# Kernel optimization log

Measured on AMD Instinct MI355X. Metric: run time of the kernel, lower is better.

The kernel has to match this reference:

```python
import jax, jax.numpy as jnp
import numpy as np

N_NODES = 50000
N_EDGES = 600000
NFEAT = 128
HIDDEN = 64
NCLASS = 40


def sage_conv(x, src, dst, Wl, bl, Wr, num_nodes):
    # PyG SAGEConv (aggr='mean'): out = lin_l(mean_{j->i} x_j) + lin_r(x_i)
    msg = x[src]                                                  # [E, d]
    agg = jax.ops.segment_sum(msg, dst, num_segments=num_nodes)   # [N, d]
    cnt = jax.ops.segment_sum(jnp.ones((src.shape[0],), x.dtype), dst,
                              num_segments=num_nodes)             # [N]
    agg = agg / jnp.maximum(cnt, 1.0)[:, None]
    return agg @ Wl.T + bl + x @ Wr.T


def setup_inputs() -> dict:
    key = jax.random.key(0)
    ks = jax.random.split(key, 8)
    x = jax.random.normal(ks[0], (N_NODES, NFEAT), dtype=jnp.float32)
    edge_index = jax.random.randint(ks[1], (2, N_EDGES), 0, N_NODES, dtype=jnp.int64)
    def glorot(k, shape):
        lim = np.sqrt(6.0 / (shape[0] + shape[1]))
        return jax.random.uniform(k, shape, jnp.float32, -lim, lim)
    Wl1 = glorot(ks[2], (HIDDEN, NFEAT))
    bl1 = jnp.zeros((HIDDEN,), jnp.float32)
    Wr1 = glorot(ks[3], (HIDDEN, NFEAT))
    Wl2 = glorot(ks[4], (NCLASS, HIDDEN))
    bl2 = jnp.zeros((NCLASS,), jnp.float32)
    Wr2 = glorot(ks[5], (NCLASS, HIDDEN))
    return {"x": x, "edge_index": edge_index, "Wl1": Wl1, "bl1": bl1,
            "Wr1": Wr1, "Wl2": Wl2, "bl2": bl2, "Wr2": Wr2}


def reference(x, edge_index, Wl1, bl1, Wr1, Wl2, bl2, Wr2):
    src, dst = edge_index[0], edge_index[1]
    h = sage_conv(x, src, dst, Wl1, bl1, Wr1, N_NODES)   # [N, 64]
    h = jax.nn.sigmoid(h)
    out = sage_conv(h, src, dst, Wl2, bl2, Wr2, N_NODES)  # [N, nclass]
    return out
```

## Files before the change

### kernel.cpp

```cpp
#include <hip/hip_runtime.h>
#include <cmath>

#define NN 50000
#define NE 600000
#define NF 128
#define NH 64
#define NC 40

#define SCAN_TPB 512
#define SCAN_NBLK 98

#define LDSP1 65
#define LDSP2 41

__global__ __launch_bounds__(256) void k_hist(const int* __restrict__ dst,
                                              int* __restrict__ deg) {
  int i0 = blockIdx.x * blockDim.x + threadIdx.x;
  int stride = gridDim.x * blockDim.x;
  for (int e = i0; e < NE; e += stride) atomicAdd(&deg[dst[e]], 1);
}

__global__ __launch_bounds__(SCAN_TPB) void k_scan1(const int* __restrict__ deg,
                                                    int* __restrict__ blocksum) {
  __shared__ int sd[SCAN_TPB];
  int i = blockIdx.x * SCAN_TPB + threadIdx.x;
  sd[threadIdx.x] = (i < NN) ? deg[i] : 0;
  __syncthreads();
  for (int off = SCAN_TPB / 2; off > 0; off >>= 1) {
    if (threadIdx.x < off) sd[threadIdx.x] += sd[threadIdx.x + off];
    __syncthreads();
  }
  if (threadIdx.x == 0) blocksum[blockIdx.x] = sd[0];
}

__global__ __launch_bounds__(128) void k_scan2(const int* __restrict__ blocksum,
                                               int* __restrict__ blockoff) {
  __shared__ int sd[128];
  int tid = threadIdx.x;
  int v = (tid < SCAN_NBLK) ? blocksum[tid] : 0;
  sd[tid] = v;
  __syncthreads();
  for (int off = 1; off < 128; off <<= 1) {
    int t = (tid >= off) ? sd[tid - off] : 0;
    __syncthreads();
    sd[tid] += t;
    __syncthreads();
  }
  if (tid < SCAN_NBLK) blockoff[tid] = sd[tid] - v;
}

__global__ __launch_bounds__(SCAN_TPB) void k_scan3(
    const int* __restrict__ deg, const int* __restrict__ blockoff,
    int* __restrict__ rowptr, int* __restrict__ cursor) {
  __shared__ int sd[SCAN_TPB];
  int tid = threadIdx.x;
  int i = blockIdx.x * SCAN_TPB + tid;
  int v = (i < NN) ? deg[i] : 0;
  sd[tid] = v;
  __syncthreads();
  for (int off = 1; off < SCAN_TPB; off <<= 1) {
    int t = (tid >= off) ? sd[tid - off] : 0;
    __syncthreads();
    sd[tid] += t;
    __syncthreads();
  }
  if (i < NN) {
    int excl = blockoff[blockIdx.x] + sd[tid] - v;
    rowptr[i] = excl;
    cursor[i] = excl;
  }
}

__global__ __launch_bounds__(256) void k_fill(const int* __restrict__ src,
                                              const int* __restrict__ dst,
                                              int* __restrict__ cursor,
                                              int* __restrict__ eid) {
  int i0 = blockIdx.x * blockDim.x + threadIdx.x;
  int stride = gridDim.x * blockDim.x;
  for (int e = i0; e < NE; e += stride) {
    int pos = atomicAdd(&cursor[dst[e]], 1);
    eid[pos] = src[e];
  }
}

__global__ __launch_bounds__(256) void k_dual_proj1(
    const float* __restrict__ X, const float* __restrict__ Wl,
    const float* __restrict__ Wr, const float* __restrict__ bl,
    float* __restrict__ P, float* __restrict__ Q) {
  __shared__ float swl[NF * LDSP1];
  __shared__ float swr[NF * LDSP1];
  int tid = threadIdx.x;
  for (int i = tid; i < NF * NH; i += 256) {
    int o = i >> 7, k = i & 127;
    swl[k * LDSP1 + o] = Wl[i];
    swr[k * LDSP1 + o] = Wr[i];
  }
  __syncthreads();
  int lane = tid & 63;
  int wave = blockIdx.x * 4 + (tid >> 6);
  int nw = gridDim.x * 4;
  float blv = bl[lane];
  const int ngroups = NN / 8;
  for (int g = wave; g < ngroups; g += nw) {
    int n0 = g * 8;
    const float4* xr = (const float4*)(X + (size_t)n0 * NF);
    float accP[8], accQ[8];
#pragma unroll
    for (int m = 0; m < 8; ++m) { accP[m] = 0.f; accQ[m] = 0.f; }
#pragma unroll 4
    for (int kk = 0; kk < 32; ++kk) {
      const float* wl4 = &swl[(kk * 4) * LDSP1 + lane];
      const float* wr4 = &swr[(kk * 4) * LDSP1 + lane];
      float l0 = wl4[0], l1 = wl4[LDSP1], l2 = wl4[2 * LDSP1], l3 = wl4[3 * LDSP1];
      float r0 = wr4[0], r1 = wr4[LDSP1], r2 = wr4[2 * LDSP1], r3 = wr4[3 * LDSP1];
#pragma unroll
      for (int m = 0; m < 8; ++m) {
        float4 v = xr[m * 32 + kk];
        accP[m] += v.x * l0 + v.y * l1 + v.z * l2 + v.w * l3;
        accQ[m] += v.x * r0 + v.y * r1 + v.z * r2 + v.w * r3;
      }
    }
#pragma unroll
    for (int m = 0; m < 8; ++m) {
      P[(size_t)(n0 + m) * NH + lane] = accP[m];
      Q[(size_t)(n0 + m) * NH + lane] = accQ[m] + blv;
    }
  }
}

__global__ __launch_bounds__(256) void k_dual_proj2(
    const float* __restrict__ H, const float* __restrict__ Wl,
    const float* __restrict__ Wr, const float* __restrict__ bl,
    float* __restrict__ P2, float* __restrict__ Q2) {
  __shared__ float swl[NH * LDSP2 + 64];
  __shared__ float swr[NH * LDSP2 + 64];
  int tid = threadIdx.x;
  for (int i = tid; i < NC * NH; i += 256) {
    int j = i >> 6, k = i & 63;
    swl[k * LDSP2 + j] = Wl[i];
    swr[k * LDSP2 + j] = Wr[i];
  }
  __syncthreads();
  int lane = tid & 63;
  int wave = blockIdx.x * 4 + (tid >> 6);
  int nw = gridDim.x * 4;
  float blv = (lane < NC) ? bl[lane] : 0.f;
  const int ngroups = NN / 8;
  for (int g = wave; g < ngroups; g += nw) {
    int n0 = g * 8;
    const float4* hr = (const float4*)(H + (size_t)n0 * NH);
    float accP[8], accQ[8];
#pragma unroll
    for (int m = 0; m < 8; ++m) { accP[m] = 0.f; accQ[m] = 0.f; }
#pragma unroll 4
    for (int kk = 0; kk < 16; ++kk) {
      const float* wl4 = &swl[(kk * 4) * LDSP2 + lane];
      const float* wr4 = &swr[(kk * 4) * LDSP2 + lane];
      float l0 = wl4[0], l1 = wl4[LDSP2], l2 = wl4[2 * LDSP2], l3 = wl4[3 * LDSP2];
      float r0 = wr4[0], r1 = wr4[LDSP2], r2 = wr4[2 * LDSP2], r3 = wr4[3 * LDSP2];
#pragma unroll
      for (int m = 0; m < 8; ++m) {
        float4 v = hr[m * 16 + kk];
        accP[m] += v.x * l0 + v.y * l1 + v.z * l2 + v.w * l3;
        accQ[m] += v.x * r0 + v.y * r1 + v.z * r2 + v.w * r3;
      }
    }
    if (lane < NC) {
#pragma unroll
      for (int m = 0; m < 8; ++m) {
        P2[(size_t)(n0 + m) * NC + lane] = accP[m];
        Q2[(size_t)(n0 + m) * NC + lane] = accQ[m] + blv;
      }
    }
  }
}

__global__ __launch_bounds__(256) void k_gather64(
    const float* __restrict__ P, const float* __restrict__ Q,
    const int* __restrict__ rowptr, const int* __restrict__ deg,
    const int* __restrict__ eid, float* __restrict__ H) {
  int lane = threadIdx.x & 63;
  int wave = blockIdx.x * 4 + (threadIdx.x >> 6);
  int nw = gridDim.x * 4;
  for (int n = wave; n < NN; n += nw) {
    int r0 = rowptr[n], dg = deg[n];
    float a0 = 0.f, a1 = 0.f;
    for (int base = 0; base < dg; base += 64) {
      int e = dg - base;
      if (e > 64) e = 64;
      int myeid = (lane < e) ? eid[r0 + base + lane] : 0;
      int j = 0;
      for (; j + 4 <= e; j += 4) {
        int s0 = __shfl(myeid, j);
        int s1 = __shfl(myeid, j + 1);
        int s2 = __shfl(myeid, j + 2);
        int s3 = __shfl(myeid, j + 3);
        float v0 = P[(size_t)s0 * NH + lane];
        float v1 = P[(size_t)s1 * NH + lane];
        float v2 = P[(size_t)s2 * NH + lane];
        float v3 = P[(size_t)s3 * NH + lane];
        a0 += v0 + v2;
        a1 += v1 + v3;
      }
      for (; j < e; ++j) a0 += P[(size_t)__shfl(myeid, j) * NH + lane];
    }
    float inv = 1.0f / (float)(dg > 0 ? dg : 1);
    float val = (a0 + a1) * inv + Q[(size_t)n * NH + lane];
    H[(size_t)n * NH + lane] = 1.0f / (1.0f + __expf(-val));
  }
}

__global__ __launch_bounds__(256) void k_gather40(
    const float* __restrict__ P2, const float* __restrict__ Q2,
    const int* __restrict__ rowptr, const int* __restrict__ deg,
    const int* __restrict__ eid, float* __restrict__ Out) {
  int lane = threadIdx.x & 63;
  int wave = blockIdx.x * 4 + (threadIdx.x >> 6);
  int nw = gridDim.x * 4;
  for (int n = wave; n < NN; n += nw) {
    int r0 = rowptr[n], dg = deg[n];
    float a0 = 0.f, a1 = 0.f;
    for (int base = 0; base < dg; base += 64) {
      int e = dg - base;
      if (e > 64) e = 64;
      int myeid = (lane < e) ? eid[r0 + base + lane] : 0;
      int j = 0;
      for (; j + 4 <= e; j += 4) {
        int s0 = __shfl(myeid, j);
        int s1 = __shfl(myeid, j + 1);
        int s2 = __shfl(myeid, j + 2);
        int s3 = __shfl(myeid, j + 3);
        if (lane < NC) {
          float v0 = P2[(size_t)s0 * NC + lane];
          float v1 = P2[(size_t)s1 * NC + lane];
          float v2 = P2[(size_t)s2 * NC + lane];
          float v3 = P2[(size_t)s3 * NC + lane];
          a0 += v0 + v2;
          a1 += v1 + v3;
        }
      }
      for (; j < e; ++j) {
        int s0 = __shfl(myeid, j);
        if (lane < NC) a0 += P2[(size_t)s0 * NC + lane];
      }
    }
    if (lane < NC) {
      float inv = 1.0f / (float)(dg > 0 ? dg : 1);
      Out[(size_t)n * NC + lane] = (a0 + a1) * inv + Q2[(size_t)n * NC + lane];
    }
  }
}

extern "C" void kernel_launch(void* const* d_in, const int* in_sizes, int n_in,
                              void* d_out, int out_size, void* d_ws,
                              size_t ws_size, hipStream_t stream) {
  const float* x = (const float*)d_in[0];
  const int* ei = (const int*)d_in[1];
  const float* Wl1 = (const float*)d_in[2];
  const float* bl1 = (const float*)d_in[3];
  const float* Wr1 = (const float*)d_in[4];
  const float* Wl2 = (const float*)d_in[5];
  const float* bl2 = (const float*)d_in[6];
  const float* Wr2 = (const float*)d_in[7];
  float* out = (float*)d_out;

  const int* src = ei;
  const int* dst = ei + NE;

  float* fws = (float*)d_ws;
  float* p1 = fws;
  float* q1 = p1 + (size_t)NN * NH;
  float* h = q1 + (size_t)NN * NH;
  float* p2 = fws;
  float* q2 = fws + (size_t)NN * NC;
  int* deg = (int*)(h + (size_t)NN * NH);
  int* rowptr = deg + NN;
  int* cursor = rowptr + NN;
  int* blocksum = cursor + NN;
  int* blockoff = blocksum + 128;
  int* eid = blockoff + 128;

  hipMemsetAsync(deg, 0, NN * sizeof(int), stream);

  k_hist<<<1024, 256, 0, stream>>>(dst, deg);
  k_scan1<<<SCAN_NBLK, SCAN_TPB, 0, stream>>>(deg, blocksum);
  k_scan2<<<1, 128, 0, stream>>>(blocksum, blockoff);
  k_scan3<<<SCAN_NBLK, SCAN_TPB, 0, stream>>>(deg, blockoff, rowptr, cursor);
  k_fill<<<1024, 256, 0, stream>>>(src, dst, cursor, eid);

  k_dual_proj1<<<512, 256, 0, stream>>>(x, Wl1, Wr1, bl1, p1, q1);
  k_gather64<<<2048, 256, 0, stream>>>(p1, q1, rowptr, deg, eid, h);

  k_dual_proj2<<<512, 256, 0, stream>>>(h, Wl2, Wr2, bl2, p2, q2);
  k_gather40<<<2048, 256, 0, stream>>>(p2, q2, rowptr, deg, eid, out);
}
```

Measured before the change: 314.9 us.

## Split layer-1 projection and vectorize gathers with half-wave float2 loads

The fused dual projection for layer 1 becomes two single-weight launches of a smaller kernel. Each uses half the LDS, which allows more blocks per CU, but X is now read twice. The two gather kernels now handle two edges per wave step: each half-wave loads float2 rows and the halves are combined with a cross-half shuffle reduction. This halves the gather loop iterations and widens the memory accesses. Grid sizes for the projections are also doubled.

Result: slower. 356.0 us (+13.0%).

```diff
diff --git a/kernel.cpp b/kernel.cpp
--- a/kernel.cpp
+++ b/kernel.cpp
@@ -83,48 +83,40 @@
   }
 }
 
-__global__ __launch_bounds__(256) void k_dual_proj1(
-    const float* __restrict__ X, const float* __restrict__ Wl,
-    const float* __restrict__ Wr, const float* __restrict__ bl,
-    float* __restrict__ P, float* __restrict__ Q) {
-  __shared__ float swl[NF * LDSP1];
-  __shared__ float swr[NF * LDSP1];
+__global__ __launch_bounds__(256) void k_proj1(
+    const float* __restrict__ X, const float* __restrict__ W,
+    const float* __restrict__ bias,
+    float* __restrict__ O) {
+  __shared__ float sw[NF * LDSP1];
   int tid = threadIdx.x;
   for (int i = tid; i < NF * NH; i += 256) {
     int o = i >> 7, k = i & 127;
-    swl[k * LDSP1 + o] = Wl[i];
-    swr[k * LDSP1 + o] = Wr[i];
+    sw[k * LDSP1 + o] = W[i];
   }
   __syncthreads();
   int lane = tid & 63;
   int wave = blockIdx.x * 4 + (tid >> 6);
   int nw = gridDim.x * 4;
-  float blv = bl[lane];
+  float bv = bias ? bias[lane] : 0.f;
   const int ngroups = NN / 8;
   for (int g = wave; g < ngroups; g += nw) {
     int n0 = g * 8;
     const float4* xr = (const float4*)(X + (size_t)n0 * NF);
-    float accP[8], accQ[8];
-#pragma unroll
-    for (int m = 0; m < 8; ++m) { accP[m] = 0.f; accQ[m] = 0.f; }
+    float acc[8];
+#pragma unroll
+    for (int m = 0; m < 8; ++m) acc[m] = 0.f;
 #pragma unroll 4
     for (int kk = 0; kk < 32; ++kk) {
-      const float* wl4 = &swl[(kk * 4) * LDSP1 + lane];
-      const float* wr4 = &swr[(kk * 4) * LDSP1 + lane];
-      float l0 = wl4[0], l1 = wl4[LDSP1], l2 = wl4[2 * LDSP1], l3 = wl4[3 * LDSP1];
-      float r0 = wr4[0], r1 = wr4[LDSP1], r2 = wr4[2 * LDSP1], r3 = wr4[3 * LDSP1];
+      const float* w4 = &sw[(kk * 4) * LDSP1 + lane];
+      float w0 = w4[0], w1 = w4[LDSP1], w2 = w4[2 * LDSP1], w3 = w4[3 * LDSP1];
 #pragma unroll
       for (int m = 0; m < 8; ++m) {
         float4 v = xr[m * 32 + kk];
-        accP[m] += v.x * l0 + v.y * l1 + v.z * l2 + v.w * l3;
-        accQ[m] += v.x * r0 + v.y * r1 + v.z * r2 + v.w * r3;
-      }
-    }
-#pragma unroll
-    for (int m = 0; m < 8; ++m) {
-      P[(size_t)(n0 + m) * NH + lane] = accP[m];
-      Q[(size_t)(n0 + m) * NH + lane] = accQ[m] + blv;
-    }
+        acc[m] += v.x * w0 + v.y * w1 + v.z * w2 + v.w * w3;
+      }
+    }
+#pragma unroll
+    for (int m = 0; m < 8; ++m) O[(size_t)(n0 + m) * NH + lane] = acc[m] + bv;
   }
 }
 
@@ -180,33 +172,46 @@
     const int* __restrict__ rowptr, const int* __restrict__ deg,
     const int* __restrict__ eid, float* __restrict__ H) {
   int lane = threadIdx.x & 63;
+  int h = lane >> 5, c2 = lane & 31;
   int wave = blockIdx.x * 4 + (threadIdx.x >> 6);
   int nw = gridDim.x * 4;
   for (int n = wave; n < NN; n += nw) {
     int r0 = rowptr[n], dg = deg[n];
-    float a0 = 0.f, a1 = 0.f;
+    float ax0 = 0.f, ay0 = 0.f, ax1 = 0.f, ay1 = 0.f;
     for (int base = 0; base < dg; base += 64) {
       int e = dg - base;
       if (e > 64) e = 64;
       int myeid = (lane < e) ? eid[r0 + base + lane] : 0;
       int j = 0;
       for (; j + 4 <= e; j += 4) {
-        int s0 = __shfl(myeid, j);
-        int s1 = __shfl(myeid, j + 1);
-        int s2 = __shfl(myeid, j + 2);
-        int s3 = __shfl(myeid, j + 3);
-        float v0 = P[(size_t)s0 * NH + lane];
-        float v1 = P[(size_t)s1 * NH + lane];
-        float v2 = P[(size_t)s2 * NH + lane];
-        float v3 = P[(size_t)s3 * NH + lane];
-        a0 += v0 + v2;
-        a1 += v1 + v3;
-      }
-      for (; j < e; ++j) a0 += P[(size_t)__shfl(myeid, j) * NH + lane];
-    }
-    float inv = 1.0f / (float)(dg > 0 ? dg : 1);
-    float val = (a0 + a1) * inv + Q[(size_t)n * NH + lane];
-    H[(size_t)n * NH + lane] = 1.0f / (1.0f + __expf(-val));
+        int sA = __shfl(myeid, j + h);
+        int sB = __shfl(myeid, j + 2 + h);
+        float2 vA = *(const float2*)(P + (size_t)sA * NH + 2 * c2);
+        float2 vB = *(const float2*)(P + (size_t)sB * NH + 2 * c2);
+        ax0 += vA.x; ay0 += vA.y;
+        ax1 += vB.x; ay1 += vB.y;
+      }
+      for (; j < e; j += 2) {
+        int sA = __shfl(myeid, j + h);
+        if (j + h < e) {
+          float2 vA = *(const float2*)(P + (size_t)sA * NH + 2 * c2);
+          ax0 += vA.x; ay0 += vA.y;
+        }
+      }
+    }
+    float sx = ax0 + ax1, sy = ay0 + ay1;
+    sx += __shfl_xor(sx, 32);
+    sy += __shfl_xor(sy, 32);
+    if (h == 0) {
+      float inv = 1.0f / (float)(dg > 0 ? dg : 1);
+      float2 qv = *(const float2*)(Q + (size_t)n * NH + 2 * c2);
+      float vx = sx * inv + qv.x;
+      float vy = sy * inv + qv.y;
+      float2 o;
+      o.x = 1.0f / (1.0f + __expf(-vx));
+      o.y = 1.0f / (1.0f + __expf(-vy));
+      *(float2*)(H + (size_t)n * NH + 2 * c2) = o;
+    }
   }
 }
 
@@ -215,38 +220,45 @@
     const int* __restrict__ rowptr, const int* __restrict__ deg,
     const int* __restrict__ eid, float* __restrict__ Out) {
   int lane = threadIdx.x & 63;
+  int h = lane >> 5, c2 = lane & 31;
   int wave = blockIdx.x * 4 + (threadIdx.x >> 6);
   int nw = gridDim.x * 4;
   for (int n = wave; n < NN; n += nw) {
     int r0 = rowptr[n], dg = deg[n];
-    float a0 = 0.f, a1 = 0.f;
+    float ax0 = 0.f, ay0 = 0.f, ax1 = 0.f, ay1 = 0.f;
     for (int base = 0; base < dg; base += 64) {
       int e = dg - base;
       if (e > 64) e = 64;
       int myeid = (lane < e) ? eid[r0 + base + lane] : 0;
       int j = 0;
       for (; j + 4 <= e; j += 4) {
-        int s0 = __shfl(myeid, j);
-        int s1 = __shfl(myeid, j + 1);
-        int s2 = __shfl(myeid, j + 2);
-        int s3 = __shfl(myeid, j + 3);
-        if (lane < NC) {
-          float v0 = P2[(size_t)s0 * NC + lane];
-          float v1 = P2[(size_t)s1 * NC + lane];
-          float v2 = P2[(size_t)s2 * NC + lane];
-          float v3 = P2[(size_t)s3 * NC + lane];
-          a0 += v0 + v2;
-          a1 += v1 + v3;
+        int sA = __shfl(myeid, j + h);
+        int sB = __shfl(myeid, j + 2 + h);
+        if (c2 < 20) {
+          float2 vA = *(const float2*)(P2 + (size_t)sA * NC + 2 * c2);
+          float2 vB = *(const float2*)(P2 + (size_t)sB * NC + 2 * c2);
+          ax0 += vA.x; ay0 += vA.y;
+          ax1 += vB.x; ay1 += vB.y;
         }
       }
-      for (; j < e; ++j) {
-        int s0 = __shfl(myeid, j);
-        if (lane < NC) a0 += P2[(size_t)s0 * NC + lane];
-      }
-    }
-    if (lane < NC) {
+      for (; j < e; j += 2) {
+        int sA = __shfl(myeid, j + h);
+        if (c2 < 20 && (j + h) < e) {
+          float2 vA = *(const float2*)(P2 + (size_t)sA * NC + 2 * c2);
+          ax0 += vA.x; ay0 += vA.y;
+        }
+      }
+    }
+    float sx = ax0 + ax1, sy = ay0 + ay1;
+    sx += __shfl_xor(sx, 32);
+    sy += __shfl_xor(sy, 32);
+    if (h == 0 && c2 < 20) {
       float inv = 1.0f / (float)(dg > 0 ? dg : 1);
-      Out[(size_t)n * NC + lane] = (a0 + a1) * inv + Q2[(size_t)n * NC + lane];
+      float2 qv = *(const float2*)(Q2 + (size_t)n * NC + 2 * c2);
+      float2 o;
+      o.x = sx * inv + qv.x;
+      o.y = sy * inv + qv.y;
+      *(float2*)(Out + (size_t)n * NC + 2 * c2) = o;
     }
   }
 }
@@ -288,9 +300,10 @@
   k_scan3<<<SCAN_NBLK, SCAN_TPB, 0, stream>>>(deg, blockoff, rowptr, cursor);
   k_fill<<<1024, 256, 0, stream>>>(src, dst, cursor, eid);
 
-  k_dual_proj1<<<512, 256, 0, stream>>>(x, Wl1, Wr1, bl1, p1, q1);
+  k_proj1<<<1024, 256, 0, stream>>>(x, Wl1, nullptr, p1);
+  k_proj1<<<1024, 256, 0, stream>>>(x, Wr1, bl1, q1);
   k_gather64<<<2048, 256, 0, stream>>>(p1, q1, rowptr, deg, eid, h);
 
-  k_dual_proj2<<<512, 256, 0, stream>>>(h, Wl2, Wr2, bl2, p2, q2);
+  k_dual_proj2<<<1024, 256, 0, stream>>>(h, Wl2, Wr2, bl2, p2, q2);
   k_gather40<<<2048, 256, 0, stream>>>(p2, q2, rowptr, deg, eid, out);
 }
```
